# Kernel optimization log

Measured on AMD Instinct MI355X. Metric: run time of the kernel, lower is better.

## Reference

```python
import jax, jax.numpy as jnp
import numpy as np

N_NODES = 50000
N_EDGES = 1600000
IN_FEATS = 256
OUT_FEATS = 64


def setup_inputs() -> dict:
    key = jax.random.key(0)
    k_x, k_w, k_b, k_s, k_d = jax.random.split(key, 5)
    x = jax.random.normal(k_x, (N_NODES, IN_FEATS), dtype=jnp.float32)
    # nn.Linear(in_feats, out_feats): weight [out, in], bias [out]
    W = jax.random.normal(k_w, (OUT_FEATS, IN_FEATS), dtype=jnp.float32) / np.sqrt(IN_FEATS)
    b = jax.random.normal(k_b, (OUT_FEATS,), dtype=jnp.float32) * 0.01
    edge_src = jax.random.randint(k_s, (N_EDGES,), 0, N_NODES, dtype=jnp.int32)
    edge_dst = jax.random.randint(k_d, (N_EDGES,), 0, N_NODES, dtype=jnp.int32)
    return {"x": x, "W": W, "b": b, "edge_src": edge_src, "edge_dst": edge_dst}


def reference(x, W, b, edge_src, edge_dst):
    # h = dropout(relu(Linear(x)))  -- dropout p=0 (eval) => identity
    h = jax.nn.relu(x @ W.T + b)                     # [N, out_feats]
    # update_all: message = h[src], reduce = mean over incoming edges per dst
    msg = h[edge_src]                                # [E, out_feats] gather
    summed = jax.ops.segment_sum(msg, edge_dst, num_segments=N_NODES)  # [N, out]
    deg = jax.ops.segment_sum(jnp.ones((edge_src.shape[0],), dtype=h.dtype),
                              edge_dst, num_segments=N_NODES)          # [N]
    deg = jnp.maximum(deg, 1.0)
    return summed / deg[:, None]
```

## Files before the change

kernel.cpp:

```cpp
#include <hip/hip_runtime.h>
#include <hip/hip_bf16.h>

#define K_IN 256
#define O_OUT 64
#define NBINS 1024
#define NPB 49
#define CAP 1824
#define PART_CHUNK 4096
#define XS_STRIDE 136

typedef __attribute__((ext_vector_type(8))) short short8;
typedef __attribute__((ext_vector_type(4))) float f32x4;

__device__ inline unsigned short bf16bits(float a) {
  __hip_bfloat16 t = __float2bfloat16(a);
  return *(unsigned short*)&t;
}

__global__ __launch_bounds__(256) void k_prep(const float* __restrict__ W,
                                              unsigned short* __restrict__ Wb,
                                              int* __restrict__ cursor) {
  int i = blockIdx.x * 256 + threadIdx.x;
  Wb[i] = bf16bits(W[i]);
  if (i < NBINS) cursor[i] = 0;
}

struct GemmSmem {
  unsigned short xs[64 * XS_STRIDE];
};
struct PartSmem {
  int cnt[NBINS];
  int scanb[NBINS];
  int gbase[NBINS];
  int wsum[4];
  unsigned ord[PART_CHUNK];
};
union FusedSmem {
  GemmSmem g;
  PartSmem p;
};

__device__ void gemm_body(GemmSmem& sm, int gid, const float* __restrict__ x,
                          const unsigned short* __restrict__ Wb,
                          const float* __restrict__ bias,
                          __hip_bfloat16* __restrict__ h, int N) {
  const int tid = threadIdx.x;
  const int lane = tid & 63;
  const int wv = tid >> 6;
  const int n0 = gid * 64;

  f32x4 acc[4] = {{0.f, 0.f, 0.f, 0.f}, {0.f, 0.f, 0.f, 0.f},
                  {0.f, 0.f, 0.f, 0.f}, {0.f, 0.f, 0.f, 0.f}};
  const unsigned short* wbase = Wb + (lane & 15) * K_IN + (lane >> 4) * 8;

  for (int kc = 0; kc < K_IN; kc += 128) {
    __syncthreads();
    unsigned* xdst = (unsigned*)sm.xs;
#pragma unroll
    for (int r = 0; r < 8; ++r) {
      int flat = r * 256 + tid;
      int row = flat >> 5;
      int c4 = flat & 31;
      float4 v = make_float4(0.f, 0.f, 0.f, 0.f);
      int node = n0 + row;
      if (node < N) v = *(const float4*)(x + (size_t)node * K_IN + kc + c4 * 4);
      unsigned u0 = (unsigned)bf16bits(v.x) | ((unsigned)bf16bits(v.y) << 16);
      unsigned u1 = (unsigned)bf16bits(v.z) | ((unsigned)bf16bits(v.w) << 16);
      xdst[row * (XS_STRIDE / 2) + c4 * 2] = u0;
      xdst[row * (XS_STRIDE / 2) + c4 * 2 + 1] = u1;
    }
    __syncthreads();

    const unsigned short* arow =
        sm.xs + (wv * 16 + (lane & 15)) * XS_STRIDE + (lane >> 4) * 8;
#pragma unroll
    for (int k0 = 0; k0 < 128; k0 += 32) {
      short8 a = *(const short8*)(arow + k0);
#pragma unroll
      for (int nt = 0; nt < 4; ++nt) {
        short8 bfr = *(const short8*)(wbase + nt * 16 * K_IN + kc + k0);
        acc[nt] = __builtin_amdgcn_mfma_f32_16x16x32_bf16(a, bfr, acc[nt], 0, 0, 0);
      }
    }
  }

  const int col = lane & 15;
  const int rbase = (lane >> 4) * 4;
#pragma unroll
  for (int nt = 0; nt < 4; ++nt) {
    float bv = bias[nt * 16 + col];
#pragma unroll
    for (int j = 0; j < 4; ++j) {
      int node = n0 + wv * 16 + rbase + j;
      if (node < N) {
        float v = fmaxf(acc[nt][j] + bv, 0.f);
        h[(size_t)node * O_OUT + nt * 16 + col] = __float2bfloat16(v);
      }
    }
  }
}

__device__ void part_body(PartSmem& sm, int pid, const int* __restrict__ esrc,
                          const int* __restrict__ edst, int* __restrict__ cursor,
                          unsigned* __restrict__ bucket, int E) {
  const int tid = threadIdx.x;
  const int lane = tid & 63;
  const int wid = tid >> 6;
  const int base = pid * PART_CHUNK;

#pragma unroll
  for (int r = 0; r < 4; ++r) sm.cnt[r * 256 + tid] = 0;
  __syncthreads();

  unsigned pk[16];
  int bn[16];
  int rk[16];
#pragma unroll
  for (int r = 0; r < 4; ++r) {
    int e0 = base + r * 1024 + tid * 4;
    int4 s4, d4;
    if (e0 + 3 < E) {
      s4 = *(const int4*)(esrc + e0);
      d4 = *(const int4*)(edst + e0);
    } else {
      s4 = make_int4(0, 0, 0, 0);
      d4 = make_int4(0, 0, 0, 0);
      int* sp = (int*)&s4;
      int* dp = (int*)&d4;
      for (int j = 0; j < 4; ++j)
        if (e0 + j < E) { sp[j] = esrc[e0 + j]; dp[j] = edst[e0 + j]; }
    }
    const int* sp = (const int*)&s4;
    const int* dp = (const int*)&d4;
#pragma unroll
    for (int j = 0; j < 4; ++j) {
      int k = r * 4 + j;
      int e = e0 + j;
      if (e < E) {
        int s = sp[j];
        int d = dp[j];
        int bb = (int)__umulhi((unsigned)d, 87652394u);
        int dl = d - bb * NPB;
        pk[k] = (unsigned)s | ((unsigned)dl << 16) | ((unsigned)bb << 22);
        bn[k] = bb;
        rk[k] = atomicAdd(&sm.cnt[bb], 1);
      } else {
        bn[k] = -1;
      }
    }
  }
  __syncthreads();

  int c0 = sm.cnt[4 * tid];
  int c1 = sm.cnt[4 * tid + 1];
  int c2 = sm.cnt[4 * tid + 2];
  int c3 = sm.cnt[4 * tid + 3];
  int s = c0 + c1 + c2 + c3;
  int incl = s;
#pragma unroll
  for (int off = 1; off < 64; off <<= 1) {
    int t = __shfl_up(incl, off);
    if (lane >= off) incl += t;
  }
  if (lane == 63) sm.wsum[wid] = incl;
  __syncthreads();
  int wpre = 0;
  for (int w = 0; w < wid; ++w) wpre += sm.wsum[w];
  int excl = wpre + incl - s;
  sm.scanb[4 * tid] = excl;
  sm.scanb[4 * tid + 1] = excl + c0;
  sm.scanb[4 * tid + 2] = excl + c0 + c1;
  sm.scanb[4 * tid + 3] = excl + c0 + c1 + c2;
  sm.gbase[4 * tid] = (c0 > 0) ? atomicAdd(&cursor[4 * tid], c0) : 0;
  sm.gbase[4 * tid + 1] = (c1 > 0) ? atomicAdd(&cursor[4 * tid + 1], c1) : 0;
  sm.gbase[4 * tid + 2] = (c2 > 0) ? atomicAdd(&cursor[4 * tid + 2], c2) : 0;
  sm.gbase[4 * tid + 3] = (c3 > 0) ? atomicAdd(&cursor[4 * tid + 3], c3) : 0;
  __syncthreads();

#pragma unroll
  for (int k = 0; k < 16; ++k) {
    if (bn[k] >= 0) {
      int pos = sm.scanb[bn[k]] + rk[k];
      sm.ord[pos] = pk[k];
    }
  }
  __syncthreads();

  int nv = E - base;
  if (nv > PART_CHUNK) nv = PART_CHUNK;
  for (int p = tid; p < nv; p += 256) {
    unsigned v = sm.ord[p];
    int bb = v >> 22;
    int slot = sm.gbase[bb] + (p - sm.scanb[bb]);
    if (slot < CAP) bucket[(size_t)bb * CAP + slot] = v;
  }
}

__global__ __launch_bounds__(256, 5) void k_fused(const float* __restrict__ x,
                                                  const unsigned short* __restrict__ Wb,
                                                  const float* __restrict__ bias,
                                                  __hip_bfloat16* __restrict__ h,
                                                  const int* __restrict__ esrc,
                                                  const int* __restrict__ edst,
                                                  int* __restrict__ cursor,
                                                  unsigned* __restrict__ bucket,
                                                  int N, int E) {
  __shared__ FusedSmem sm;
  const int npart = (E + PART_CHUNK - 1) / PART_CHUNK;
  const int b = blockIdx.x;
  if (b % 3 == 1 && b / 3 < npart) {
    part_body(sm.p, b / 3, esrc, edst, cursor, bucket, E);
  } else {
    int skipped = (b + 2) / 3;
    if (skipped > npart) skipped = npart;
    gemm_body(sm.g, b - skipped, x, Wb, bias, h, N);
  }
}

__global__ __launch_bounds__(512) void k_sortagg(const unsigned* __restrict__ bucket,
                                                 const int* __restrict__ cursor,
                                                 const unsigned* __restrict__ h32,
                                                 float* __restrict__ out, int N) {
  __shared__ int hist[NPB];
  __shared__ int offs[NPB];
  __shared__ unsigned short sbuf[CAP + 64];

  const int tid = threadIdx.x;
  const int lane = tid & 63;
  const int wid = tid >> 6;
  const int bin = blockIdx.x;

  if (tid < NPB) hist[tid] = 0;
  __syncthreads();

  int cnt = cursor[bin];
  if (cnt > CAP) cnt = CAP;
  const unsigned* bb = bucket + (size_t)bin * CAP;

  unsigned pk[4];
  int rk[4];
  {
    int i0 = tid * 4;
    uint4 v;
    if (i0 + 3 < cnt) {
      v = *(const uint4*)(bb + i0);
    } else {
      v = make_uint4(0, 0, 0, 0);
      unsigned* vp = (unsigned*)&v;
      for (int j = 0; j < 4; ++j)
        if (i0 + j < cnt) vp[j] = bb[i0 + j];
    }
    const unsigned* vp = (const unsigned*)&v;
#pragma unroll
    for (int j = 0; j < 4; ++j) {
      if (i0 + j < cnt) {
        pk[j] = vp[j];
        rk[j] = atomicAdd(&hist[(vp[j] >> 16) & 63], 1);
      } else {
        rk[j] = -1;
      }
    }
  }
  __syncthreads();

  if (tid < 64) {
    int hval = (tid < NPB) ? hist[tid] : 0;
    int incl = hval;
#pragma unroll
    for (int off = 1; off < 64; off <<= 1) {
      int t = __shfl_up(incl, off);
      if (lane >= off) incl += t;
    }
    if (tid < NPB) offs[tid] = incl - hval;
  }
  __syncthreads();

#pragma unroll
  for (int j = 0; j < 4; ++j) {
    if (rk[j] >= 0)
      sbuf[offs[(pk[j] >> 16) & 63] + rk[j]] = (unsigned short)(pk[j] & 0xFFFFu);
  }
  __syncthreads();

  const int q = lane >> 4;
  const int hl = lane & 15;
  const uint2* __restrict__ h2 = (const uint2*)h32;

  for (int nl = wid; nl < NPB; nl += 8) {
    int n = bin * NPB + nl;
    if (n >= N) break;
    int c = hist[nl];
    const unsigned short* bs = sbuf + offs[nl];

    float a0 = 0.f, a1 = 0.f, a2 = 0.f, a3 = 0.f;
    const int nqc = (c + 3) >> 2;
    for (int i0 = 0; i0 < nqc; i0 += 8) {
      int p[8];
#pragma unroll
      for (int k = 0; k < 8; ++k) {
        int e = (i0 + k) * 4 + q;
        p[k] = (e < c) ? (int)bs[e] : 0;
      }
#pragma unroll
      for (int k = 0; k < 8; ++k) {
        float wk = ((i0 + k) * 4 + q < c) ? 1.f : 0.f;
        uint2 u = h2[p[k] * 16 + hl];
        a0 = fmaf(wk, __uint_as_float(u.x << 16), a0);
        a1 = fmaf(wk, __uint_as_float(u.x & 0xFFFF0000u), a1);
        a2 = fmaf(wk, __uint_as_float(u.y << 16), a2);
        a3 = fmaf(wk, __uint_as_float(u.y & 0xFFFF0000u), a3);
      }
    }

    a0 += __shfl_xor(a0, 16); a1 += __shfl_xor(a1, 16);
    a2 += __shfl_xor(a2, 16); a3 += __shfl_xor(a3, 16);
    a0 += __shfl_xor(a0, 32); a1 += __shfl_xor(a1, 32);
    a2 += __shfl_xor(a2, 32); a3 += __shfl_xor(a3, 32);

    if (lane < 16) {
      float inv = 1.f / fmaxf((float)c, 1.f);
      float4 r;
      r.x = a0 * inv; r.y = a1 * inv; r.z = a2 * inv; r.w = a3 * inv;
      *(float4*)(out + (size_t)n * O_OUT + hl * 4) = r;
    }
  }
}

extern "C" void kernel_launch(void* const* d_in, const int* in_sizes, int n_in,
                              void* d_out, int out_size, void* d_ws, size_t ws_size,
                              hipStream_t stream) {
  const float* x = (const float*)d_in[0];
  const float* W = (const float*)d_in[1];
  const float* b = (const float*)d_in[2];
  const int* esrc = (const int*)d_in[3];
  const int* edst = (const int*)d_in[4];
  float* out = (float*)d_out;

  const int N = in_sizes[0] / K_IN;
  const int E = in_sizes[3];

  char* ws = (char*)d_ws;
  unsigned short* Wb = (unsigned short*)ws;
  __hip_bfloat16* h = (__hip_bfloat16*)(ws + 32768);
  size_t off = 32768 + (size_t)N * O_OUT * sizeof(__hip_bfloat16);
  int* cursor = (int*)(ws + off);
  off += NBINS * sizeof(int);
  unsigned* bucket = (unsigned*)(ws + off);

  const int ngemm = (N + 63) / 64;
  const int npart = (E + PART_CHUNK - 1) / PART_CHUNK;

  k_prep<<<(K_IN * O_OUT) / 256, 256, 0, stream>>>(W, Wb, cursor);
  k_fused<<<ngemm + npart, 256, 0, stream>>>(x, Wb, b, h, esrc, edst, cursor,
                                             bucket, N, E);
  k_sortagg<<<NBINS, 512, 0, stream>>>(bucket, cursor, (const unsigned*)h, out, N);
}
```

Measured before the change: 174.8 us.

## Stage swizzled bf16 weights in LDS and stream x directly from global

The GEMM phase now loads the full bf16 weight matrix into LDS once, using an XOR swizzle to avoid bank conflicts. Each lane then reads its x row fragments straight from global memory and converts them to bf16 in registers before the MFMAs. This drops the per-chunk x staging and the barriers between chunks. In exchange, x loads are less coalesced (strided per-lane reads), and the shared-memory union grows to 32KB, which could lower occupancy for the fused kernel.

```diff
diff --git a/kernel.cpp b/kernel.cpp
--- a/kernel.cpp
+++ b/kernel.cpp
@@ -7,7 +7,6 @@
 #define NPB 49
 #define CAP 1824
 #define PART_CHUNK 4096
-#define XS_STRIDE 136
 
 typedef __attribute__((ext_vector_type(8))) short short8;
 typedef __attribute__((ext_vector_type(4))) float f32x4;
@@ -15,6 +14,15 @@
 __device__ inline unsigned short bf16bits(float a) {
   __hip_bfloat16 t = __float2bfloat16(a);
   return *(unsigned short*)&t;
+}
+
+__device__ inline short8 cvt8(float4 f0, float4 f1) {
+  short8 r;
+  r[0] = (short)bf16bits(f0.x); r[1] = (short)bf16bits(f0.y);
+  r[2] = (short)bf16bits(f0.z); r[3] = (short)bf16bits(f0.w);
+  r[4] = (short)bf16bits(f1.x); r[5] = (short)bf16bits(f1.y);
+  r[6] = (short)bf16bits(f1.z); r[7] = (short)bf16bits(f1.w);
+  return r;
 }
 
 __global__ __launch_bounds__(256) void k_prep(const float* __restrict__ W,
@@ -26,7 +34,7 @@
 }
 
 struct GemmSmem {
-  unsigned short xs[64 * XS_STRIDE];
+  unsigned short wsb[64 * 256];
 };
 struct PartSmem {
   int cnt[NBINS];
@@ -49,38 +57,42 @@
   const int wv = tid >> 6;
   const int n0 = gid * 64;
 
-  f32x4 acc[4] = {{0.f, 0.f, 0.f, 0.f}, {0.f, 0.f, 0.f, 0.f},
-                  {0.f, 0.f, 0.f, 0.f}, {0.f, 0.f, 0.f, 0.f}};
-  const unsigned short* wbase = Wb + (lane & 15) * K_IN + (lane >> 4) * 8;
-
-  for (int kc = 0; kc < K_IN; kc += 128) {
-    __syncthreads();
-    unsigned* xdst = (unsigned*)sm.xs;
+  {
+    const uint4* wsrc = (const uint4*)Wb;
 #pragma unroll
     for (int r = 0; r < 8; ++r) {
       int flat = r * 256 + tid;
       int row = flat >> 5;
-      int c4 = flat & 31;
-      float4 v = make_float4(0.f, 0.f, 0.f, 0.f);
-      int node = n0 + row;
-      if (node < N) v = *(const float4*)(x + (size_t)node * K_IN + kc + c4 * 4);
-      unsigned u0 = (unsigned)bf16bits(v.x) | ((unsigned)bf16bits(v.y) << 16);
-      unsigned u1 = (unsigned)bf16bits(v.z) | ((unsigned)bf16bits(v.w) << 16);
-      xdst[row * (XS_STRIDE / 2) + c4 * 2] = u0;
-      xdst[row * (XS_STRIDE / 2) + c4 * 2 + 1] = u1;
-    }
-    __syncthreads();
-
-    const unsigned short* arow =
-        sm.xs + (wv * 16 + (lane & 15)) * XS_STRIDE + (lane >> 4) * 8;
-#pragma unroll
-    for (int k0 = 0; k0 < 128; k0 += 32) {
-      short8 a = *(const short8*)(arow + k0);
-#pragma unroll
-      for (int nt = 0; nt < 4; ++nt) {
-        short8 bfr = *(const short8*)(wbase + nt * 16 * K_IN + kc + k0);
-        acc[nt] = __builtin_amdgcn_mfma_f32_16x16x32_bf16(a, bfr, acc[nt], 0, 0, 0);
-      }
+      int c16 = flat & 31;
+      unsigned byte = (unsigned)(row * 512 + c16 * 16);
+      byte ^= (unsigned)((row & 7) << 4);
+      *(uint4*)((char*)sm.wsb + byte) = wsrc[flat];
+    }
+  }
+
+  f32x4 acc[4] = {{0.f, 0.f, 0.f, 0.f}, {0.f, 0.f, 0.f, 0.f},
+                  {0.f, 0.f, 0.f, 0.f}, {0.f, 0.f, 0.f, 0.f}};
+
+  int anode = n0 + wv * 16 + (lane & 15);
+  if (anode > N - 1) anode = N - 1;
+  const float* aptr = x + (size_t)anode * K_IN + (lane >> 4) * 8;
+  const int brow0 = lane & 15;
+  const unsigned kb = (unsigned)((lane >> 4) * 16);
+  const unsigned bswz = (unsigned)((brow0 & 7) << 4);
+
+  __syncthreads();
+
+#pragma unroll
+  for (int k = 0; k < K_IN; k += 32) {
+    float4 f0 = *(const float4*)(aptr + k);
+    float4 f1 = *(const float4*)(aptr + k + 4);
+    short8 a = cvt8(f0, f1);
+#pragma unroll
+    for (int nt = 0; nt < 4; ++nt) {
+      unsigned byte = (unsigned)((brow0 + nt * 16) * 512 + k * 2) + kb;
+      byte ^= bswz;
+      short8 bfr = *(const short8*)((const char*)sm.wsb + byte);
+      acc[nt] = __builtin_amdgcn_mfma_f32_16x16x32_bf16(a, bfr, acc[nt], 0, 0, 0);
     }
   }
 
```

After: 160.8 us. 1.09x faster.
